# Kernel optimization log

Measured on AMD Instinct MI355X. Metric: run time of the kernel, lower is better.

Reference implementation:

```python
import jax, jax.numpy as jnp
import numpy as np

NUM_HEADS = 16

def setup_inputs() -> dict:
    key = jax.random.key(0)
    k1, k2, k3 = jax.random.split(key, 3)
    B, N, C = 2, 2048, 1024
    x = jax.random.normal(k1, (B, N, C), dtype=jnp.float32)
    w_qkv = jax.random.normal(k2, (C, 3 * C), dtype=jnp.float32) * (C ** -0.5)
    w_proj = jax.random.normal(k3, (C, C), dtype=jnp.float32) * (C ** -0.5)
    b_proj = jnp.zeros((C,), dtype=jnp.float32)
    return {"x": x, "w_qkv": w_qkv, "w_proj": w_proj, "b_proj": b_proj}

def reference(x, w_qkv, w_proj, b_proj):
    B, N, C = x.shape
    H = NUM_HEADS
    D = C // H
    scale = D ** -0.5
    qkv = (x @ w_qkv).reshape(B, N, 3, H, D).transpose(2, 0, 3, 1, 4)  # [3,B,H,N,D]
    q, k, v = qkv[0], qkv[1], qkv[2]
    attn = jnp.einsum("bhnd,bhmd->bhnm", q, k) * scale  # [B,H,N,N]
    attn = jax.nn.softmax(attn, axis=-1)
    out = jnp.einsum("bhnm,bhmd->bhnd", attn, v)  # [B,H,N,D]
    out = out.transpose(0, 2, 1, 3).reshape(B, N, C)
    return out @ w_proj + b_proj
```

## Files before the change

### kernel.cpp

```cpp
#include <hip/hip_runtime.h>
#include <hip/hip_bf16.h>
#include <math.h>

#define B_SZ   2
#define N_SEQ  2048
#define C_DIM  1024
#define H_NUM  16
#define D_HEAD 64
#define M_ROWS (B_SZ * N_SEQ)
#define QKV_N  (3 * C_DIM)

typedef __attribute__((ext_vector_type(8))) short  bf16x8;
typedef __attribute__((ext_vector_type(4))) float  floatx4;

static __device__ __forceinline__ unsigned short f2bf(float x) {
    unsigned int u = __float_as_uint(x);
    u = (u + 0x7FFFu + ((u >> 16) & 1u)) >> 16;
    return (unsigned short)u;
}
static __device__ __forceinline__ unsigned int f2bf_hi(float x) {
    unsigned int u = __float_as_uint(x);
    return u + 0x7FFFu + ((u >> 16) & 1u);
}
#if __has_builtin(__builtin_amdgcn_cvt_pk_bf16_f32)
typedef __bf16 bf16_2 __attribute__((ext_vector_type(2)));
static __device__ __forceinline__ unsigned int pkbf(float a, float b) {
    union { bf16_2 v; unsigned int u; } c;
    c.v = __builtin_amdgcn_cvt_pk_bf16_f32(a, b);
    return c.u;
}
#else
static __device__ __forceinline__ unsigned int pkbf(float a, float b) {
    return __builtin_amdgcn_perm(f2bf_hi(b), f2bf_hi(a), 0x07060302u);
}
#endif

#if __has_builtin(__builtin_amdgcn_exp2f)
#define EXP2F(x) __builtin_amdgcn_exp2f(x)
#else
#define EXP2F(x) exp2f(x)
#endif

#define GLP(p) ((const __attribute__((address_space(1))) void*)(p))
#define LDP(p) ((__attribute__((address_space(3))) void*)(p))

#define CEXP 0.18033688011112042f

__global__ __launch_bounds__(256)
void prep_fused(const float* __restrict__ x,      unsigned short* __restrict__ xb,
                const float* __restrict__ w_qkv,  unsigned short* __restrict__ wqkvT,
                const float* __restrict__ w_proj, unsigned short* __restrict__ wprojT)
{
    __shared__ unsigned short t[64][72];
    const int bid = blockIdx.x;
    const int tid = threadIdx.x;

    if (bid < 4096) {
        const int i = bid * 256 + tid;
        float4 v = ((const float4*)x)[i];
        ushort4 p;
        p.x = f2bf(v.x); p.y = f2bf(v.y); p.z = f2bf(v.z); p.w = f2bf(v.w);
        ((ushort4*)xb)[i] = p;
        return;
    }

    const float* W;
    unsigned short* WT;
    int N, tt;
    if (bid < 4096 + 768) { W = w_qkv;  WT = wqkvT;  N = QKV_N; tt = bid - 4096; }
    else                  { W = w_proj; WT = wprojT; N = C_DIM; tt = bid - 4864; }
    const int ntiles = N / 64;
    const int n0 = (tt % ntiles) * 64;
    const int k0 = (tt / ntiles) * 64;
    const int K  = C_DIM;

    const int tc = tid & 15;
    const int tr = tid >> 4;
    #pragma unroll
    for (int p = 0; p < 4; ++p) {
        const int r = tr + p * 16;
        float4 v = *(const float4*)&W[(size_t)(k0 + r) * N + n0 + tc * 4];
        ushort4 pk;
        pk.x = f2bf(v.x); pk.y = f2bf(v.y); pk.z = f2bf(v.z); pk.w = f2bf(v.w);
        *(ushort4*)&t[r][tc * 4] = pk;
    }
    __syncthreads();

    const int n  = tid >> 2;
    const int c0 = (tid & 3) * 16;
    unsigned short tmp[16];
    #pragma unroll
    for (int i = 0; i < 16; ++i) tmp[i] = t[c0 + i][n];
    *(uint4*)&WT[(size_t)(n0 + n) * K + k0 + c0]     = *(uint4*)&tmp[0];
    *(uint4*)&WT[(size_t)(n0 + n) * K + k0 + c0 + 8] = *(uint4*)&tmp[8];
}

__global__ __launch_bounds__(256)
void gemm_qkv(const unsigned short* __restrict__ A,
              const unsigned short* __restrict__ BT,
              unsigned short* __restrict__ qbuf,
              unsigned short* __restrict__ kbuf,
              unsigned short* __restrict__ vbuf)
{
    const int K = C_DIM;
    __shared__ unsigned short As[128 * 64];
    __shared__ unsigned short Bs[128 * 64];

    const int tid  = threadIdx.x;
    const int lane = tid & 63;
    const int wave = tid >> 6;
    const int l15  = lane & 15;
    const int lq   = lane >> 4;
    const int e7   = l15 & 7;
    const int wm   = (wave & 1) * 64;
    const int wn   = (wave >> 1) * 64;

    const int bid = blockIdx.x;
    const int xcd = bid & 7;
    const int j   = bid >> 3;
    const int bm  = (j / 3) * 128;
    const int bn  = ((j % 3) * 8 + xcd) * 128;

    const int srow = tid >> 3;
    const int gso  = ((tid & 7) ^ (srow & 7)) * 8;

    const unsigned short* ga = A  + (size_t)(bm + srow) * K + gso;
    const unsigned short* gb = BT + (size_t)(bn + srow) * K + gso;

    floatx4 acc[4][4];
    #pragma unroll
    for (int i = 0; i < 4; ++i)
        #pragma unroll
        for (int jj = 0; jj < 4; ++jj) acc[i][jj] = (floatx4){0.f, 0.f, 0.f, 0.f};

    for (int kt = 0; kt < K; kt += 64) {
        #pragma unroll
        for (int i = 0; i < 4; ++i) {
            __builtin_amdgcn_global_load_lds(GLP(ga + (size_t)i * 32 * K + kt),
                                             LDP(&As[i * 2048 + tid * 8]), 16, 0, 0);
            __builtin_amdgcn_global_load_lds(GLP(gb + (size_t)i * 32 * K + kt),
                                             LDP(&Bs[i * 2048 + tid * 8]), 16, 0, 0);
        }
        __syncthreads();

        bf16x8 af[2][4], bfr[2][4];
        #pragma unroll
        for (int t = 0; t < 4; ++t) {
            #pragma unroll
            for (int kc = 0; kc < 2; ++kc) {
                af[kc][t]  = *(const bf16x8*)&As[(wm + t * 16 + l15) * 64
                                                 + (((kc * 4 + lq) ^ e7) * 8)];
                bfr[kc][t] = *(const bf16x8*)&Bs[(wn + t * 16 + l15) * 64
                                                 + (((kc * 4 + lq) ^ e7) * 8)];
            }
        }
        #pragma unroll
        for (int kc = 0; kc < 2; ++kc)
            #pragma unroll
            for (int mt = 0; mt < 4; ++mt)
                #pragma unroll
                for (int nt = 0; nt < 4; ++nt)
                    acc[mt][nt] = __builtin_amdgcn_mfma_f32_16x16x32_bf16(
                        af[kc][mt], bfr[kc][nt], acc[mt][nt], 0, 0, 0);
        __syncthreads();
    }

    #pragma unroll
    for (int nt = 0; nt < 4; ++nt) {
        const int col  = bn + wn + nt * 16 + l15;
        const int reg3 = col >> 10;
        const int h    = (col >> 6) & 15;
        const int d    = col & 63;
        const float sc4 = (reg3 == 0) ? CEXP : 1.0f;
        #pragma unroll
        for (int mt = 0; mt < 4; ++mt) {
            const int row = bm + wm + mt * 16 + lq * 4;
            const int b   = row >> 11;
            const int n   = row & 2047;
            if (reg3 < 2) {
                unsigned short* dst = (reg3 ? kbuf : qbuf)
                    + ((size_t)(b * H_NUM + h) * N_SEQ + n) * D_HEAD + d;
                #pragma unroll
                for (int r = 0; r < 4; ++r)
                    dst[(size_t)r * D_HEAD] = f2bf(acc[mt][nt][r] * sc4);
            } else {
                const int a  = n & 63;
                const int fk = (a & 0x20) | ((a & 0x0C) << 1) | ((a & 0x10) >> 2);
                unsigned short* dst = vbuf
                    + ((size_t)(b * H_NUM + h) * D_HEAD + d) * N_SEQ + (n & ~63) + fk;
                ushort4 pk;
                pk.x = f2bf(acc[mt][nt][0]); pk.y = f2bf(acc[mt][nt][1]);
                pk.z = f2bf(acc[mt][nt][2]); pk.w = f2bf(acc[mt][nt][3]);
                *(ushort4*)dst = pk;
            }
        }
    }
}

__global__ __launch_bounds__(256)
void attn_mfma(const unsigned short* __restrict__ qbuf,
               const unsigned short* __restrict__ kbuf,
               const unsigned short* __restrict__ vbuf,
               unsigned short* __restrict__ attnb)
{
    __shared__ unsigned short KsS[2][64 * 64];
    __shared__ unsigned short VtS[2][64 * 64];

    const int tid  = threadIdx.x;
    const int lane = tid & 63;
    const int wave = tid >> 6;
    const int l15  = lane & 15;
    const int lq   = lane >> 4;
    const int e    = l15 & 7;

    const int bid  = blockIdx.x;
    const int bh   = (bid & 7) * 4 + (bid >> 7);
    const int qblk = (bid >> 3) & 15;
    const int b    = bh >> 4;
    const int h    = bh & 15;
    const int q0   = qblk * 128 + wave * 32;

    const unsigned short* khead = kbuf + (size_t)bh * N_SEQ * D_HEAD;
    const unsigned short* vhead = vbuf + (size_t)bh * D_HEAD * N_SEQ;

    bf16x8 qf[2][2];
    #pragma unroll
    for (int qb = 0; qb < 2; ++qb) {
        const unsigned short* qrow = qbuf
            + ((size_t)bh * N_SEQ + q0 + qb * 16 + l15) * D_HEAD + lq * 8;
        qf[0][qb] = *(const bf16x8*)qrow;
        qf[1][qb] = *(const bf16x8*)(qrow + 32);
    }

    floatx4 acc[4][2];
    #pragma unroll
    for (int dc = 0; dc < 4; ++dc)
        #pragma unroll
        for (int qb = 0; qb < 2; ++qb) acc[dc][qb] = (floatx4){0.f, 0.f, 0.f, 0.f};
    float lsum[2] = {0.f, 0.f};

    const int srow = tid >> 3;
    const int gso  = ((tid & 7) ^ (srow & 7)) * 8;

    #pragma unroll
    for (int i = 0; i < 2; ++i) {
        __builtin_amdgcn_global_load_lds(GLP(khead + (size_t)(i * 32 + srow) * 64 + gso),
                                         LDP(&KsS[0][i * 2048 + tid * 8]), 16, 0, 0);
        __builtin_amdgcn_global_load_lds(GLP(vhead + (size_t)(i * 32 + srow) * N_SEQ + gso),
                                         LDP(&VtS[0][i * 2048 + tid * 8]), 16, 0, 0);
    }

    for (int tile = 0; tile < N_SEQ / 64; ++tile) {
        const int cur = tile & 1;
        __syncthreads();

        if (tile + 1 < N_SEQ / 64) {
            const int m1 = (tile + 1) * 64;
            const int nx = cur ^ 1;
            #pragma unroll
            for (int i = 0; i < 2; ++i) {
                __builtin_amdgcn_global_load_lds(
                    GLP(khead + (size_t)(m1 + i * 32 + srow) * 64 + gso),
                    LDP(&KsS[nx][i * 2048 + tid * 8]), 16, 0, 0);
                __builtin_amdgcn_global_load_lds(
                    GLP(vhead + (size_t)(i * 32 + srow) * N_SEQ + m1 + gso),
                    LDP(&VtS[nx][i * 2048 + tid * 8]), 16, 0, 0);
            }
        }

        const unsigned short* Ksc = &KsS[cur][0];
        const unsigned short* Vtc = &VtS[cur][0];

        floatx4 st[4][2];
        #pragma unroll
        for (int t = 0; t < 4; ++t) {
            bf16x8 k0 = *(const bf16x8*)&Ksc[(t * 16 + l15) * 64 + ((lq ^ e) * 8)];
            bf16x8 k1 = *(const bf16x8*)&Ksc[(t * 16 + l15) * 64 + (((4 + lq) ^ e) * 8)];
            #pragma unroll
            for (int qb = 0; qb < 2; ++qb) {
                floatx4 s = (floatx4){-8.f, -8.f, -8.f, -8.f};
                s = __builtin_amdgcn_mfma_f32_16x16x32_bf16(k0, qf[0][qb], s, 0, 0, 0);
                s = __builtin_amdgcn_mfma_f32_16x16x32_bf16(k1, qf[1][qb], s, 0, 0, 0);
                st[t][qb] = s;
            }
        }

        bf16x8 pf[2][2];
        #pragma unroll
        for (int qb = 0; qb < 2; ++qb) {
            unsigned int pk[8];
            float la = 0.f;
            #pragma unroll
            for (int t = 0; t < 4; ++t) {
                float p0 = EXP2F(st[t][qb][0]);
                float p1 = EXP2F(st[t][qb][1]);
                float p2 = EXP2F(st[t][qb][2]);
                float p3 = EXP2F(st[t][qb][3]);
                la += (p0 + p1) + (p2 + p3);
                pk[t * 2]     = pkbf(p0, p1);
                pk[t * 2 + 1] = pkbf(p2, p3);
            }
            lsum[qb] += la;
            union { uint4 u; bf16x8 v; } c0, c1;
            c0.u = make_uint4(pk[0], pk[1], pk[2], pk[3]);
            c1.u = make_uint4(pk[4], pk[5], pk[6], pk[7]);
            pf[0][qb] = c0.v;
            pf[1][qb] = c1.v;
        }

        #pragma unroll
        for (int dc = 0; dc < 4; ++dc) {
            bf16x8 v0 = *(const bf16x8*)&Vtc[(dc * 16 + l15) * 64 + ((lq ^ e) * 8)];
            bf16x8 v1 = *(const bf16x8*)&Vtc[(dc * 16 + l15) * 64 + (((4 + lq) ^ e) * 8)];
            #pragma unroll
            for (int qb = 0; qb < 2; ++qb) {
                acc[dc][qb] = __builtin_amdgcn_mfma_f32_16x16x32_bf16(
                    v0, pf[0][qb], acc[dc][qb], 0, 0, 0);
                acc[dc][qb] = __builtin_amdgcn_mfma_f32_16x16x32_bf16(
                    v1, pf[1][qb], acc[dc][qb], 0, 0, 0);
            }
        }
    }

    #pragma unroll
    for (int qb = 0; qb < 2; ++qb) {
        float l = lsum[qb];
        l += __shfl_xor(l, 16, 64);
        l += __shfl_xor(l, 32, 64);
        const float inv = 1.f / l;
        const int q = q0 + qb * 16 + l15;
        unsigned short* orow = attnb + ((size_t)b * N_SEQ + q) * C_DIM + h * D_HEAD;
        #pragma unroll
        for (int dc = 0; dc < 4; ++dc) {
            ushort4 pkk;
            pkk.x = f2bf(acc[dc][qb][0] * inv);
            pkk.y = f2bf(acc[dc][qb][1] * inv);
            pkk.z = f2bf(acc[dc][qb][2] * inv);
            pkk.w = f2bf(acc[dc][qb][3] * inv);
            *(ushort4*)&orow[dc * 16 + lq * 4] = pkk;
        }
    }
}

__global__ __launch_bounds__(256)
void gemm_bt(const unsigned short* __restrict__ A,
             const unsigned short* __restrict__ BT,
             const float* __restrict__ bias,
             float* __restrict__ Cm,
             int M, int N, int K)
{
    __shared__ unsigned short As[128 * 64];
    __shared__ unsigned short Bs[64 * 64];

    const int tid  = threadIdx.x;
    const int lane = tid & 63;
    const int wave = tid >> 6;
    const int l15  = lane & 15;
    const int lq   = lane >> 4;
    const int e7   = l15 & 7;
    const int wm   = (wave & 1) * 64;
    const int wn   = (wave >> 1) * 32;

    const int bid = blockIdx.x;
    const int xcd = bid & 7;
    const int j   = bid >> 3;
    const int bm  = (j >> 1) * 128;
    const int bn  = ((j & 1) * 8 + xcd) * 64;

    const int srow = tid >> 3;
    const int gso  = ((tid & 7) ^ (srow & 7)) * 8;

    const unsigned short* ga = A  + (size_t)(bm + srow) * K + gso;
    const unsigned short* gb = BT + (size_t)(bn + srow) * K + gso;

    floatx4 acc[4][2];
    #pragma unroll
    for (int i = 0; i < 4; ++i)
        #pragma unroll
        for (int jj = 0; jj < 2; ++jj) acc[i][jj] = (floatx4){0.f, 0.f, 0.f, 0.f};

    for (int kt = 0; kt < K; kt += 64) {
        #pragma unroll
        for (int i = 0; i < 4; ++i)
            __builtin_amdgcn_global_load_lds(GLP(ga + (size_t)i * 32 * K + kt),
                                             LDP(&As[i * 2048 + tid * 8]), 16, 0, 0);
        #pragma unroll
        for (int i = 0; i < 2; ++i)
            __builtin_amdgcn_global_load_lds(GLP(gb + (size_t)i * 32 * K + kt),
                                             LDP(&Bs[i * 2048 + tid * 8]), 16, 0, 0);
        __syncthreads();

        bf16x8 af[2][4], bfr[2][2];
        #pragma unroll
        for (int t = 0; t < 4; ++t)
            #pragma unroll
            for (int kc = 0; kc < 2; ++kc)
                af[kc][t] = *(const bf16x8*)&As[(wm + t * 16 + l15) * 64
                                                + (((kc * 4 + lq) ^ e7) * 8)];
        #pragma unroll
        for (int t = 0; t < 2; ++t)
            #pragma unroll
            for (int kc = 0; kc < 2; ++kc)
                bfr[kc][t] = *(const bf16x8*)&Bs[(wn + t * 16 + l15) * 64
                                                 + (((kc * 4 + lq) ^ e7) * 8)];
        #pragma unroll
        for (int kc = 0; kc < 2; ++kc)
            #pragma unroll
            for (int mt = 0; mt < 4; ++mt)
                #pragma unroll
                for (int nt = 0; nt < 2; ++nt)
                    acc[mt][nt] = __builtin_amdgcn_mfma_f32_16x16x32_bf16(
                        af[kc][mt], bfr[kc][nt], acc[mt][nt], 0, 0, 0);
        __syncthreads();
    }

    float bv[2];
    #pragma unroll
    for (int nt = 0; nt < 2; ++nt) bv[nt] = bias[bn + wn + nt * 16 + l15];
    #pragma unroll
    for (int mt = 0; mt < 4; ++mt) {
        const int row = bm + wm + mt * 16 + lq * 4;
        #pragma unroll
        for (int nt = 0; nt < 2; ++nt) {
            const int col = bn + wn + nt * 16 + l15;
            #pragma unroll
            for (int r = 0; r < 4; ++r)
                Cm[(size_t)(row + r) * N + col] = acc[mt][nt][r] + bv[nt];
        }
    }
}

extern "C" void kernel_launch(void* const* d_in, const int* in_sizes, int n_in,
                              void* d_out, int out_size, void* d_ws, size_t ws_size,
                              hipStream_t stream)
{
    const float* x      = (const float*)d_in[0];
    const float* w_qkv  = (const float*)d_in[1];
    const float* w_proj = (const float*)d_in[2];
    const float* b_proj = (const float*)d_in[3];
    float*       out    = (float*)d_out;

    unsigned short* xb     = (unsigned short*)d_ws;
    unsigned short* wqkvT  = xb     + (size_t)M_ROWS * C_DIM;
    unsigned short* wprojT = wqkvT  + (size_t)QKV_N * C_DIM;
    unsigned short* qbuf   = wprojT + (size_t)C_DIM * C_DIM;
    unsigned short* kbuf   = qbuf   + (size_t)M_ROWS * C_DIM;
    unsigned short* vbuf   = kbuf   + (size_t)M_ROWS * C_DIM;
    unsigned short* attnb  = vbuf   + (size_t)M_ROWS * C_DIM;

    prep_fused<<<4096 + 768 + 256, 256, 0, stream>>>(x, xb, w_qkv, wqkvT, w_proj, wprojT);

    gemm_qkv<<<768, 256, 0, stream>>>(xb, wqkvT, qbuf, kbuf, vbuf);

    attn_mfma<<<512, 256, 0, stream>>>(qbuf, kbuf, vbuf, attnb);

    gemm_bt<<<512, 256, 0, stream>>>(attnb, wprojT, b_proj, out, M_ROWS, C_DIM, C_DIM);
}
```

Baseline: 198.4 us.

## Split attention KV sequence across two wave groups per block with LDS reduction

The attention kernel now runs 512 threads per block. Two groups of four waves each process alternating 64-key halves of a 128-key stage, so the same query tile is covered with twice the waves. The partial accumulators and row sums are then merged through shared memory before normalisation. This is meant to raise occupancy and latency hiding, and to halve the number of barriers per key. The cost is double the LDS footprint, an extra reduction step, and launch bounds that may constrain registers.

```diff
diff --git a/kernel.cpp b/kernel.cpp
--- a/kernel.cpp
+++ b/kernel.cpp
@@ -197,18 +197,20 @@
     }
 }
 
-__global__ __launch_bounds__(256)
+__global__ __launch_bounds__(512, 4)
 void attn_mfma(const unsigned short* __restrict__ qbuf,
                const unsigned short* __restrict__ kbuf,
                const unsigned short* __restrict__ vbuf,
                unsigned short* __restrict__ attnb)
 {
-    __shared__ unsigned short KsS[2][64 * 64];
-    __shared__ unsigned short VtS[2][64 * 64];
+    __shared__ unsigned short KsS[2][2][64 * 64];
+    __shared__ unsigned short VtS[2][2][64 * 64];
 
     const int tid  = threadIdx.x;
     const int lane = tid & 63;
     const int wave = tid >> 6;
+    const int grp  = wave >> 2;
+    const int wrow = wave & 3;
     const int l15  = lane & 15;
     const int lq   = lane >> 4;
     const int e    = l15 & 7;
@@ -218,7 +220,7 @@
     const int qblk = (bid >> 3) & 15;
     const int b    = bh >> 4;
     const int h    = bh & 15;
-    const int q0   = qblk * 128 + wave * 32;
+    const int q0   = qblk * 128 + wrow * 32;
 
     const unsigned short* khead = kbuf + (size_t)bh * N_SEQ * D_HEAD;
     const unsigned short* vhead = vbuf + (size_t)bh * D_HEAD * N_SEQ;
@@ -244,32 +246,32 @@
 
     #pragma unroll
     for (int i = 0; i < 2; ++i) {
-        __builtin_amdgcn_global_load_lds(GLP(khead + (size_t)(i * 32 + srow) * 64 + gso),
-                                         LDP(&KsS[0][i * 2048 + tid * 8]), 16, 0, 0);
-        __builtin_amdgcn_global_load_lds(GLP(vhead + (size_t)(i * 32 + srow) * N_SEQ + gso),
-                                         LDP(&VtS[0][i * 2048 + tid * 8]), 16, 0, 0);
-    }
-
-    for (int tile = 0; tile < N_SEQ / 64; ++tile) {
-        const int cur = tile & 1;
+        __builtin_amdgcn_global_load_lds(GLP(khead + (size_t)(i * 64 + srow) * 64 + gso),
+                                         LDP(&KsS[0][i][tid * 8]), 16, 0, 0);
+        __builtin_amdgcn_global_load_lds(GLP(vhead + (size_t)srow * N_SEQ + i * 64 + gso),
+                                         LDP(&VtS[0][i][tid * 8]), 16, 0, 0);
+    }
+
+    for (int s = 0; s < N_SEQ / 128; ++s) {
+        const int cur = s & 1;
         __syncthreads();
 
-        if (tile + 1 < N_SEQ / 64) {
-            const int m1 = (tile + 1) * 64;
+        if (s + 1 < N_SEQ / 128) {
+            const int m1 = (s + 1) * 128;
             const int nx = cur ^ 1;
             #pragma unroll
             for (int i = 0; i < 2; ++i) {
                 __builtin_amdgcn_global_load_lds(
-                    GLP(khead + (size_t)(m1 + i * 32 + srow) * 64 + gso),
-                    LDP(&KsS[nx][i * 2048 + tid * 8]), 16, 0, 0);
+                    GLP(khead + (size_t)(m1 + i * 64 + srow) * 64 + gso),
+                    LDP(&KsS[nx][i][tid * 8]), 16, 0, 0);
                 __builtin_amdgcn_global_load_lds(
-                    GLP(vhead + (size_t)(i * 32 + srow) * N_SEQ + m1 + gso),
-                    LDP(&VtS[nx][i * 2048 + tid * 8]), 16, 0, 0);
-            }
-        }
-
-        const unsigned short* Ksc = &KsS[cur][0];
-        const unsigned short* Vtc = &VtS[cur][0];
+                    GLP(vhead + (size_t)srow * N_SEQ + m1 + i * 64 + gso),
+                    LDP(&VtS[nx][i][tid * 8]), 16, 0, 0);
+            }
+        }
+
+        const unsigned short* Ksc = &KsS[cur][grp][0];
+        const unsigned short* Vtc = &VtS[cur][grp][0];
 
         floatx4 st[4][2];
         #pragma unroll
@@ -278,10 +280,10 @@
             bf16x8 k1 = *(const bf16x8*)&Ksc[(t * 16 + l15) * 64 + (((4 + lq) ^ e) * 8)];
             #pragma unroll
             for (int qb = 0; qb < 2; ++qb) {
-                floatx4 s = (floatx4){-8.f, -8.f, -8.f, -8.f};
-                s = __builtin_amdgcn_mfma_f32_16x16x32_bf16(k0, qf[0][qb], s, 0, 0, 0);
-                s = __builtin_amdgcn_mfma_f32_16x16x32_bf16(k1, qf[1][qb], s, 0, 0, 0);
-                st[t][qb] = s;
+                floatx4 sv = (floatx4){-8.f, -8.f, -8.f, -8.f};
+                sv = __builtin_amdgcn_mfma_f32_16x16x32_bf16(k0, qf[0][qb], sv, 0, 0, 0);
+                sv = __builtin_amdgcn_mfma_f32_16x16x32_bf16(k1, qf[1][qb], sv, 0, 0, 0);
+                st[t][qb] = sv;
             }
         }
 
@@ -320,6 +322,38 @@
                     v1, pf[1][qb], acc[dc][qb], 0, 0, 0);
             }
         }
+    }
+
+    __syncthreads();
+    float* smA = (float*)&KsS[0][0][0];
+    float* smL = (float*)&VtS[0][0][0];
+    const int li = wrow * 64 + lane;
+    if (grp) {
+        float* p = smA + li * 32;
+        #pragma unroll
+        for (int dc = 0; dc < 4; ++dc)
+            #pragma unroll
+            for (int qb = 0; qb < 2; ++qb)
+                #pragma unroll
+                for (int r = 0; r < 4; ++r)
+                    p[(dc * 8 + qb * 4 + r) ^ (lane & 31)] = acc[dc][qb][r];
+        smL[li * 2]     = lsum[0];
+        smL[li * 2 + 1] = lsum[1];
+    }
+    __syncthreads();
+    if (grp) return;
+
+    {
+        const float* p = smA + li * 32;
+        #pragma unroll
+        for (int dc = 0; dc < 4; ++dc)
+            #pragma unroll
+            for (int qb = 0; qb < 2; ++qb)
+                #pragma unroll
+                for (int r = 0; r < 4; ++r)
+                    acc[dc][qb][r] += p[(dc * 8 + qb * 4 + r) ^ (lane & 31)];
+        lsum[0] += smL[li * 2];
+        lsum[1] += smL[li * 2 + 1];
     }
 
     #pragma unroll
@@ -452,7 +486,7 @@
 
     gemm_qkv<<<768, 256, 0, stream>>>(xb, wqkvT, qbuf, kbuf, vbuf);
 
-    attn_mfma<<<512, 256, 0, stream>>>(qbuf, kbuf, vbuf, attnb);
+    attn_mfma<<<512, 512, 0, stream>>>(qbuf, kbuf, vbuf, attnb);
 
     gemm_bt<<<512, 256, 0, stream>>>(attnb, wprojT, b_proj, out, M_ROWS, C_DIM, C_DIM);
 }
```

Result: faster. 185.2 us (median of 2 runs) (-6.6%).
